# Optimization experiments

Hardware: AMD Instinct MI355X
Metric: run time of the kernel (lower is better)

## Reference

```python
import jax, jax.numpy as jnp
import numpy as np

N = 50000      # nodes
E = 1600000    # edges
D = 64         # in_channels (== hidden so layers stack)
H = 64         # hidden_channels
L = 3          # num_layers
G = 128        # graphs in batch
OUT = 1        # out_channels
BN_EPS = 1e-5


def setup_inputs() -> dict:
    key = jax.random.key(0)
    ks = jax.random.split(key, 8)
    s = 0.1
    x = jax.random.normal(ks[0], (N, D), dtype=jnp.float32)
    edge_index = jax.random.randint(ks[1], (2, E), 0, N, dtype=jnp.int64)
    batch = jnp.sort(jax.random.randint(ks[2], (N,), 0, G, dtype=jnp.int64))
    # stacked GINConv MLP params: Linear(D,H) -> BN(H) -> ReLU -> Linear(H,H)
    W1 = jax.random.normal(ks[3], (L, D, H), dtype=jnp.float32) * s
    b1 = jnp.zeros((L, H), jnp.float32)
    gamma = jnp.ones((L, H), jnp.float32)
    beta = jnp.zeros((L, H), jnp.float32)
    W2 = jax.random.normal(ks[4], (L, H, H), dtype=jnp.float32) * s
    b2 = jnp.zeros((L, H), jnp.float32)
    # head MLP: Linear(H,H) -> ReLU -> (dropout, eval mode) -> Linear(H,OUT)
    Wh1 = jax.random.normal(ks[5], (H, H), dtype=jnp.float32) * s
    bh1 = jnp.zeros((H,), jnp.float32)
    Wh2 = jax.random.normal(ks[6], (H, OUT), dtype=jnp.float32) * s
    bh2 = jnp.zeros((OUT,), jnp.float32)
    return dict(x=x, edge_index=edge_index, batch=batch,
                W1=W1, b1=b1, gamma=gamma, beta=beta, W2=W2, b2=b2,
                Wh1=Wh1, bh1=bh1, Wh2=Wh2, bh2=bh2)


def reference(x, edge_index, batch, W1, b1, gamma, beta, W2, b2, Wh1, bh1, Wh2, bh2):
    src, dst = edge_index[0], edge_index[1]

    def gin_layer(h, p):
        w1, bb1, g, be, w2, bb2 = p
        # scatter-add neighbor aggregation: sum_{j->i} h_j
        agg = jax.ops.segment_sum(h[src], dst, num_segments=N)  # [N, H]
        z = (agg + h) @ w1 + bb1  # (1+eps)*x + agg, eps=0; then Linear
        # BatchNorm1d (training-mode batch stats, biased var)
        mu = z.mean(0)
        var = ((z - mu) ** 2).mean(0)
        z = (z - mu) * jax.lax.rsqrt(var + BN_EPS) * g + be
        z = jax.nn.relu(z) @ w2 + bb2  # ReLU -> Linear (plain last layer)
        return jax.nn.relu(z), None    # outer .relu() in GIN.forward

    h, _ = jax.lax.scan(gin_layer, x, (W1, b1, gamma, beta, W2, b2))

    # global_mean_pool over batch ids
    cnt = jax.ops.segment_sum(jnp.ones((N, 1), h.dtype), batch, num_segments=G)
    pooled = jax.ops.segment_sum(h, batch, num_segments=G) / jnp.maximum(cnt, 1.0)

    # head MLP (dropout = identity in eval mode)
    return jax.nn.relu(pooled @ Wh1 + bh1) @ Wh2 + bh2
```

## Files before the change

### kernel.cpp

```cpp
#include <hip/hip_runtime.h>

#define N_NODES 50000
#define N_EDGES 1600000
#define HDIM 64
#define NLAYERS 3
#define NGRAPH 128
#define BN_EPS 1e-5f
#define CAP 96
#define NBINS 196
#define NBLK 782

__device__ __forceinline__ unsigned short f2bf(float f) {
    union { float f; unsigned u; } v; v.f = f;
    unsigned r = v.u + 0x7fffu + ((v.u >> 16) & 1u);
    return (unsigned short)(r >> 16);
}
__device__ __forceinline__ unsigned pack2(float a, float b) {
    return (unsigned)f2bf(a) | ((unsigned)f2bf(b) << 16);
}
__device__ __forceinline__ float bf2f(unsigned short b) {
    union { unsigned u; float f; } v; v.u = ((unsigned)b) << 16; return v.f;
}
__device__ __forceinline__ void acc8(float* a, uint4 v) {
    union { unsigned u; float f; } t;
    t.u = v.x << 16;         a[0] += t.f;
    t.u = v.x & 0xffff0000u; a[1] += t.f;
    t.u = v.y << 16;         a[2] += t.f;
    t.u = v.y & 0xffff0000u; a[3] += t.f;
    t.u = v.z << 16;         a[4] += t.f;
    t.u = v.z & 0xffff0000u; a[5] += t.f;
    t.u = v.w << 16;         a[6] += t.f;
    t.u = v.w & 0xffff0000u; a[7] += t.f;
}

__global__ __launch_bounds__(256) void hist1_kernel(
    const int* __restrict__ dst, int* __restrict__ gh)
{
    __shared__ int lh[NBINS];
    int tid = threadIdx.x;
    for (int i = tid; i < NBINS; i += 256) lh[i] = 0;
    __syncthreads();
    int t8 = blockIdx.x * 256 + tid;
    if (t8 < N_EDGES / 8) {
        int4 d0 = ((const int4*)dst)[t8 * 2];
        int4 d1 = ((const int4*)dst)[t8 * 2 + 1];
        atomicAdd(&lh[d0.x >> 8], 1);
        atomicAdd(&lh[d0.y >> 8], 1);
        atomicAdd(&lh[d0.z >> 8], 1);
        atomicAdd(&lh[d0.w >> 8], 1);
        atomicAdd(&lh[d1.x >> 8], 1);
        atomicAdd(&lh[d1.y >> 8], 1);
        atomicAdd(&lh[d1.z >> 8], 1);
        atomicAdd(&lh[d1.w >> 8], 1);
    }
    __syncthreads();
    for (int i = tid; i < NBINS; i += 256)
        gh[i * NBLK + blockIdx.x] = lh[i];
}

__global__ __launch_bounds__(256) void scan_bins_kernel(
    int* __restrict__ gh, int* __restrict__ binbase)
{
    __shared__ int wsum[4];
    __shared__ int woff[4];
    __shared__ int carry;
    int b = blockIdx.x;
    int tid = threadIdx.x, lane = tid & 63, wid = tid >> 6;
    if (tid == 0) carry = 0;
    __syncthreads();
    int* row = gh + b * NBLK;
    for (int base = 0; base < NBLK; base += 256) {
        int i = base + tid;
        int v = (i < NBLK) ? row[i] : 0;
        int incl = v;
        #pragma unroll
        for (int off = 1; off < 64; off <<= 1) {
            int t = __shfl_up(incl, off, 64);
            if (lane >= off) incl += t;
        }
        if (lane == 63) wsum[wid] = incl;
        __syncthreads();
        if (tid == 0) {
            int r = carry;
            #pragma unroll
            for (int w = 0; w < 4; ++w) { woff[w] = r; r += wsum[w]; }
            carry = r;
        }
        __syncthreads();
        if (i < NBLK) row[i] = woff[wid] + incl - v;
        __syncthreads();
    }
    if (tid == 0) binbase[b] = carry;
}

__global__ __launch_bounds__(256) void scan_base_kernel(int* __restrict__ binbase)
{
    __shared__ int wsum[4];
    __shared__ int woff[5];
    int tid = threadIdx.x, lane = tid & 63, wid = tid >> 6;
    int v = (tid < NBINS) ? binbase[tid] : 0;
    int incl = v;
    #pragma unroll
    for (int off = 1; off < 64; off <<= 1) {
        int t = __shfl_up(incl, off, 64);
        if (lane >= off) incl += t;
    }
    if (lane == 63) wsum[wid] = incl;
    __syncthreads();
    if (tid == 0) {
        int r = 0;
        #pragma unroll
        for (int w = 0; w < 4; ++w) { woff[w] = r; r += wsum[w]; }
        woff[4] = r;
    }
    __syncthreads();
    if (tid < NBINS) binbase[tid] = woff[wid] + incl - v;
    if (tid == 0) binbase[NBINS] = woff[4];
}

__global__ __launch_bounds__(256) void scatter_kernel(
    const int* __restrict__ src, const int* __restrict__ dst,
    const int* __restrict__ gh, const int* __restrict__ binbase,
    unsigned* __restrict__ packed)
{
    __shared__ int lbase[NBINS];
    int tid = threadIdx.x;
    for (int i = tid; i < NBINS; i += 256)
        lbase[i] = binbase[i] + gh[i * NBLK + blockIdx.x];
    __syncthreads();
    int t8 = blockIdx.x * 256 + tid;
    if (t8 >= N_EDGES / 8) return;
    int4 d0 = ((const int4*)dst)[t8 * 2];
    int4 d1 = ((const int4*)dst)[t8 * 2 + 1];
    int4 s0 = ((const int4*)src)[t8 * 2];
    int4 s1 = ((const int4*)src)[t8 * 2 + 1];
    int p0 = atomicAdd(&lbase[d0.x >> 8], 1);
    int p1 = atomicAdd(&lbase[d0.y >> 8], 1);
    int p2 = atomicAdd(&lbase[d0.z >> 8], 1);
    int p3 = atomicAdd(&lbase[d0.w >> 8], 1);
    int p4 = atomicAdd(&lbase[d1.x >> 8], 1);
    int p5 = atomicAdd(&lbase[d1.y >> 8], 1);
    int p6 = atomicAdd(&lbase[d1.z >> 8], 1);
    int p7 = atomicAdd(&lbase[d1.w >> 8], 1);
    packed[p0] = ((unsigned)d0.x << 16) | (unsigned)s0.x;
    packed[p1] = ((unsigned)d0.y << 16) | (unsigned)s0.y;
    packed[p2] = ((unsigned)d0.z << 16) | (unsigned)s0.z;
    packed[p3] = ((unsigned)d0.w << 16) | (unsigned)s0.w;
    packed[p4] = ((unsigned)d1.x << 16) | (unsigned)s1.x;
    packed[p5] = ((unsigned)d1.y << 16) | (unsigned)s1.y;
    packed[p6] = ((unsigned)d1.z << 16) | (unsigned)s1.z;
    packed[p7] = ((unsigned)d1.w << 16) | (unsigned)s1.w;
}

__global__ __launch_bounds__(256) void build_csr_kernel(
    const unsigned* __restrict__ packed, const int* __restrict__ binbase,
    unsigned short* __restrict__ col, int* __restrict__ cnt)
{
    __shared__ int lcnt[256];
    int b = blockIdx.x;
    int tid = threadIdx.x;
    lcnt[tid] = 0;
    __syncthreads();
    int e0 = binbase[b], e1 = binbase[b + 1];
    for (int e = e0 + tid; e < e1; e += 256) {
        unsigned p = packed[e];
        int d = (int)(p >> 16);
        int dl = d - (b << 8);
        int pos = atomicAdd(&lcnt[dl], 1);
        col[d * CAP + pos] = (unsigned short)(p & 0xffffu);
    }
    __syncthreads();
    int node = (b << 8) + tid;
    if (node < N_NODES) {
        int c = lcnt[tid];
        int end = (c + 7) & ~7;
        unsigned short* cp = col + node * CAP;
        for (int i = c; i < end; ++i) cp[i] = (unsigned short)N_NODES;
        cnt[node] = c;
    }
}

__global__ __launch_bounds__(256) void xcast_kernel(
    const float* __restrict__ x, unsigned short* __restrict__ xb)
{
    int t = blockIdx.x * 256 + threadIdx.x;
    if (t < 8)
        ((uint4*)(xb + (size_t)N_NODES * HDIM))[t] = make_uint4(0, 0, 0, 0);
    if (t >= N_NODES * HDIM / 8) return;
    float4 v0 = ((const float4*)x)[t * 2];
    float4 v1 = ((const float4*)x)[t * 2 + 1];
    uint4 o;
    o.x = pack2(v0.x, v0.y);
    o.y = pack2(v0.z, v0.w);
    o.z = pack2(v1.x, v1.y);
    o.w = pack2(v1.z, v1.w);
    ((uint4*)xb)[t] = o;
}

__global__ __launch_bounds__(256) void gather_kernel(
    const unsigned short* __restrict__ hin, const int* __restrict__ cnt,
    const unsigned short* __restrict__ col, float* __restrict__ agg)
{
    const uint4* hin4 = (const uint4*)hin;
    int row = blockIdx.x * 4 + (threadIdx.x >> 6);
    int lane = threadIdx.x & 63;
    int sub = lane >> 3;
    int q = lane & 7;
    int nch = (cnt[row] + 7) >> 3;
    const unsigned short* cp = col + row * CAP + sub;
    float a[8] = {0.f, 0.f, 0.f, 0.f, 0.f, 0.f, 0.f, 0.f};
    int ch = 0;
    for (; ch + 4 <= nch; ch += 4) {
        int c0 = cp[ch * 8];
        int c1 = cp[ch * 8 + 8];
        int c2 = cp[ch * 8 + 16];
        int c3 = cp[ch * 8 + 24];
        uint4 v0 = hin4[c0 * 8 + q];
        uint4 v1 = hin4[c1 * 8 + q];
        uint4 v2 = hin4[c2 * 8 + q];
        uint4 v3 = hin4[c3 * 8 + q];
        acc8(a, v0); acc8(a, v1); acc8(a, v2); acc8(a, v3);
    }
    if (ch + 2 <= nch) {
        int c0 = cp[ch * 8];
        int c1 = cp[ch * 8 + 8];
        uint4 v0 = hin4[c0 * 8 + q];
        uint4 v1 = hin4[c1 * 8 + q];
        acc8(a, v0); acc8(a, v1);
        ch += 2;
    }
    if (ch < nch) {
        int c0 = cp[ch * 8];
        uint4 v0 = hin4[c0 * 8 + q];
        acc8(a, v0);
    }
    #pragma unroll
    for (int off = 8; off < 64; off <<= 1) {
        #pragma unroll
        for (int j = 0; j < 8; ++j)
            a[j] += __shfl_xor(a[j], off, 64);
    }
    if (sub == 0) {
        uint4 sv = hin4[row * 8 + q];
        acc8(a, sv);
        float4 o0, o1;
        o0.x = a[0]; o0.y = a[1]; o0.z = a[2]; o0.w = a[3];
        o1.x = a[4]; o1.y = a[5]; o1.z = a[6]; o1.w = a[7];
        float4* op = (float4*)(agg + (size_t)row * HDIM + q * 8);
        op[0] = o0;
        op[1] = o1;
    }
}

__global__ __launch_bounds__(256) void gemm1_kernel(
    const float* __restrict__ agg, const float* __restrict__ W1,
    const float* __restrict__ b1, float* __restrict__ z,
    float* __restrict__ stats )
{
    __shared__ float sW[HDIM * HDIM];
    __shared__ float sIn[64][HDIM];
    __shared__ float sRedS[4][HDIM];
    __shared__ float sRedQ[4][HDIM];
    int tid = threadIdx.x;
    int w = tid >> 6, c = tid & 63;
    int row0 = blockIdx.x * 64;
    for (int i = tid; i < HDIM * HDIM; i += 256) sW[i] = W1[i];
    const float4* agg4 = (const float4*)agg;
    #pragma unroll
    for (int i = 0; i < 4; ++i) {
        int lin = tid + i * 256;
        int rr = lin >> 4, q = lin & 15;
        float4 v = (row0 + rr < N_NODES)
                       ? agg4[(size_t)(row0 + rr) * 16 + q]
                       : make_float4(0.f, 0.f, 0.f, 0.f);
        *(float4*)&sIn[rr][q * 4] = v;
    }
    float bias = b1[c];
    __syncthreads();
    float acc[16];
    #pragma unroll
    for (int r = 0; r < 16; ++r) acc[r] = bias;
    #pragma unroll 4
    for (int k4 = 0; k4 < HDIM; k4 += 4) {
        float w0 = sW[(k4 + 0) * HDIM + c];
        float w1 = sW[(k4 + 1) * HDIM + c];
        float w2 = sW[(k4 + 2) * HDIM + c];
        float w3 = sW[(k4 + 3) * HDIM + c];
        #pragma unroll
        for (int r = 0; r < 16; ++r) {
            float4 iv = *(const float4*)&sIn[w * 16 + r][k4];
            acc[r] = fmaf(iv.x, w0, acc[r]);
            acc[r] = fmaf(iv.y, w1, acc[r]);
            acc[r] = fmaf(iv.z, w2, acc[r]);
            acc[r] = fmaf(iv.w, w3, acc[r]);
        }
    }
    float s = 0.f, s2 = 0.f;
    #pragma unroll
    for (int r = 0; r < 16; ++r) {
        int row = row0 + w * 16 + r;
        if (row < N_NODES) {
            z[(size_t)row * HDIM + c] = acc[r];
            s += acc[r];
            s2 += acc[r] * acc[r];
        }
    }
    sRedS[w][c] = s;
    sRedQ[w][c] = s2;
    __syncthreads();
    if (tid < HDIM) {
        atomicAdd(&stats[c], sRedS[0][c] + sRedS[1][c] + sRedS[2][c] + sRedS[3][c]);
        atomicAdd(&stats[HDIM + c],
                  sRedQ[0][c] + sRedQ[1][c] + sRedQ[2][c] + sRedQ[3][c]);
    }
}

__global__ __launch_bounds__(256) void gemm2_kernel(
    const float* __restrict__ z, const float* __restrict__ W2,
    const float* __restrict__ b2, const float* __restrict__ stats,
    const float* __restrict__ gamma, const float* __restrict__ beta,
    unsigned short* __restrict__ hout)
{
    __shared__ float sW[HDIM * HDIM];
    __shared__ float sIn[64][HDIM];
    __shared__ float sSc[HDIM];
    __shared__ float sSh[HDIM];
    int tid = threadIdx.x;
    int w = tid >> 6, c = tid & 63;
    int row0 = blockIdx.x * 64;
    for (int i = tid; i < HDIM * HDIM; i += 256) sW[i] = W2[i];
    if (tid < HDIM) {
        float mu  = stats[tid] / (float)N_NODES;
        float var = stats[HDIM + tid] / (float)N_NODES - mu * mu;
        float sc  = gamma[tid] * rsqrtf(var + BN_EPS);
        sSc[tid] = sc;
        sSh[tid] = beta[tid] - mu * sc;
    }
    float bias = b2[c];
    __syncthreads();
    const float4* z4 = (const float4*)z;
    #pragma unroll
    for (int i = 0; i < 4; ++i) {
        int lin = tid + i * 256;
        int rr = lin >> 4, q = lin & 15;
        float4 v = (row0 + rr < N_NODES)
                       ? z4[(size_t)(row0 + rr) * 16 + q]
                       : make_float4(0.f, 0.f, 0.f, 0.f);
        int cb = q * 4;
        v.x = fmaxf(fmaf(v.x, sSc[cb + 0], sSh[cb + 0]), 0.f);
        v.y = fmaxf(fmaf(v.y, sSc[cb + 1], sSh[cb + 1]), 0.f);
        v.z = fmaxf(fmaf(v.z, sSc[cb + 2], sSh[cb + 2]), 0.f);
        v.w = fmaxf(fmaf(v.w, sSc[cb + 3], sSh[cb + 3]), 0.f);
        *(float4*)&sIn[rr][q * 4] = v;
    }
    __syncthreads();
    float acc[16];
    #pragma unroll
    for (int r = 0; r < 16; ++r) acc[r] = bias;
    #pragma unroll 4
    for (int k4 = 0; k4 < HDIM; k4 += 4) {
        float w0 = sW[(k4 + 0) * HDIM + c];
        float w1 = sW[(k4 + 1) * HDIM + c];
        float w2 = sW[(k4 + 2) * HDIM + c];
        float w3 = sW[(k4 + 3) * HDIM + c];
        #pragma unroll
        for (int r = 0; r < 16; ++r) {
            float4 iv = *(const float4*)&sIn[w * 16 + r][k4];
            acc[r] = fmaf(iv.x, w0, acc[r]);
            acc[r] = fmaf(iv.y, w1, acc[r]);
            acc[r] = fmaf(iv.z, w2, acc[r]);
            acc[r] = fmaf(iv.w, w3, acc[r]);
        }
    }
    #pragma unroll
    for (int r = 0; r < 16; ++r) {
        int row = row0 + w * 16 + r;
        if (row < N_NODES)
            hout[(size_t)row * HDIM + c] = f2bf(fmaxf(acc[r], 0.f));
    }
}

__global__ __launch_bounds__(256) void bounds_kernel(
    const int* __restrict__ batch, int* __restrict__ gstart,
    unsigned short* __restrict__ hA)
{
    int i = blockIdx.x * 256 + threadIdx.x;
    if (i < 8)
        ((uint4*)(hA + (size_t)N_NODES * HDIM))[i] = make_uint4(0, 0, 0, 0);
    if (i >= N_NODES) return;
    int g1 = batch[i];
    int g0 = (i == 0) ? -1 : batch[i - 1];
    for (int g = g0 + 1; g <= g1; ++g) gstart[g] = i;
    if (i == N_NODES - 1)
        for (int g = g1 + 1; g <= NGRAPH; ++g) gstart[g] = N_NODES;
}

__global__ __launch_bounds__(256) void pool_head_kernel(
    const unsigned short* __restrict__ h, const int* __restrict__ gstart,
    const float* __restrict__ Wh1, const float* __restrict__ bh1,
    const float* __restrict__ Wh2, const float* __restrict__ bh2,
    float* __restrict__ out)
{
    __shared__ float sW[HDIM * HDIM];
    __shared__ float sRed[4][HDIM];
    __shared__ float sMean[HDIM];
    int tid = threadIdx.x;
    int r = tid >> 6, c = tid & 63;
    int g = blockIdx.x;
    for (int i = tid; i < HDIM * HDIM; i += 256) sW[i] = Wh1[i];
    int s0 = gstart[g], s1 = gstart[g + 1];
    float acc = 0.f;
    for (int row = s0 + r; row < s1; row += 4)
        acc += bf2f(h[(size_t)row * HDIM + c]);
    sRed[r][c] = acc;
    __syncthreads();
    if (r == 0) {
        float cntf = (float)(s1 - s0);
        sMean[c] = (sRed[0][c] + sRed[1][c] + sRed[2][c] + sRed[3][c]) /
                   fmaxf(cntf, 1.0f);
    }
    __syncthreads();
    if (r == 0) {
        float a = bh1[c];
        #pragma unroll
        for (int k = 0; k < HDIM; ++k)
            a = fmaf(sMean[k], sW[k * HDIM + c], a);
        a = fmaxf(a, 0.f);
        float p = a * Wh2[c];
        #pragma unroll
        for (int off = 32; off > 0; off >>= 1)
            p += __shfl_down(p, off, 64);
        if (c == 0) out[g] = p + bh2[0];
    }
}

extern "C" void kernel_launch(void* const* d_in, const int* in_sizes, int n_in,
                              void* d_out, int out_size, void* d_ws, size_t ws_size,
                              hipStream_t stream)
{
    const float* x     = (const float*)d_in[0];
    const int*   ei    = (const int*)d_in[1];
    const int*   batch = (const int*)d_in[2];
    const float* W1    = (const float*)d_in[3];
    const float* b1    = (const float*)d_in[4];
    const float* gamma = (const float*)d_in[5];
    const float* beta  = (const float*)d_in[6];
    const float* W2    = (const float*)d_in[7];
    const float* b2    = (const float*)d_in[8];
    const float* Wh1   = (const float*)d_in[9];
    const float* bh1   = (const float*)d_in[10];
    const float* Wh2   = (const float*)d_in[11];
    const float* bh2   = (const float*)d_in[12];
    float* out = (float*)d_out;

    float*          ws  = (float*)d_ws;
    float*          hB  = ws;
    unsigned short* hA  = (unsigned short*)(hB + (size_t)N_NODES * HDIM);
    unsigned short* xb  = hA + (size_t)(N_NODES + 1) * HDIM;
    int*   gstart  = (int*)(xb + (size_t)(N_NODES + 1) * HDIM + 32);
    int*   cnt     = gstart + NGRAPH + 1;
    float* stats   = (float*)(cnt + N_NODES);
    unsigned short* col = (unsigned short*)(stats + 3 * 2 * HDIM);
    unsigned* packed = (unsigned*)(col + (size_t)N_NODES * CAP);
    int*   gh      = (int*)(packed + N_EDGES);
    int*   binbase = gh + NBINS * NBLK;

    const int* src = ei;
    const int* dst = ei + N_EDGES;

    int gemmGrid   = (N_NODES + 63) / 64;
    int gatherGrid = N_NODES / 4;
    int nodeGrid   = (N_NODES + 255) / 256;
    int castGrid   = (N_NODES * HDIM / 8 + 255) / 256;

    hipMemsetAsync(stats, 0, 3 * 2 * HDIM * sizeof(float), stream);
    hist1_kernel<<<NBLK, 256, 0, stream>>>(dst, gh);
    scan_bins_kernel<<<NBINS, 256, 0, stream>>>(gh, binbase);
    scan_base_kernel<<<1, 256, 0, stream>>>(binbase);
    scatter_kernel<<<NBLK, 256, 0, stream>>>(src, dst, gh, binbase, packed);
    build_csr_kernel<<<NBINS, 256, 0, stream>>>(packed, binbase, col, cnt);
    xcast_kernel<<<castGrid, 256, 0, stream>>>(x, xb);
    bounds_kernel<<<nodeGrid, 256, 0, stream>>>(batch, gstart, hA);

    for (int l = 0; l < NLAYERS; ++l) {
        const unsigned short* hin = (l == 0) ? xb : hA;
        float* statsl = stats + l * 2 * HDIM;
        gather_kernel<<<gatherGrid, 256, 0, stream>>>(hin, cnt, col, hB);
        gemm1_kernel<<<gemmGrid, 256, 0, stream>>>(
            hB, W1 + l * HDIM * HDIM, b1 + l * HDIM, hB , statsl);
        gemm2_kernel<<<gemmGrid, 256, 0, stream>>>(
            hB, W2 + l * HDIM * HDIM, b2 + l * HDIM, statsl,
            gamma + l * HDIM, beta + l * HDIM, hA);
    }

    pool_head_kernel<<<NGRAPH, 256, 0, stream>>>(hA, gstart, Wh1, bh1, Wh2, bh2, out);
}
```

Baseline: 335.5 us.

## Fuse neighbor gather into first GEMM kernel, staging aggregates in shared memory

The separate gather kernel is removed. Each wave of the first GEMM kernel now aggregates the neighbor features for its own 16 rows and writes them straight into the shared-memory input tile. This avoids writing the fp32 aggregate buffer to global memory and reading it back, and drops one launch per layer. In exchange the gather runs with far fewer concurrent waves, each handling rows one after another, which may hurt latency hiding for the random feature loads. Rows past the node count in the last block are no longer zero-filled in shared memory.

```diff
diff --git a/kernel.cpp b/kernel.cpp
--- a/kernel.cpp
+++ b/kernel.cpp
@@ -197,63 +197,9 @@
     ((uint4*)xb)[t] = o;
 }
 
-__global__ __launch_bounds__(256) void gather_kernel(
+__global__ __launch_bounds__(256) void gather_gemm1_kernel(
     const unsigned short* __restrict__ hin, const int* __restrict__ cnt,
-    const unsigned short* __restrict__ col, float* __restrict__ agg)
-{
-    const uint4* hin4 = (const uint4*)hin;
-    int row = blockIdx.x * 4 + (threadIdx.x >> 6);
-    int lane = threadIdx.x & 63;
-    int sub = lane >> 3;
-    int q = lane & 7;
-    int nch = (cnt[row] + 7) >> 3;
-    const unsigned short* cp = col + row * CAP + sub;
-    float a[8] = {0.f, 0.f, 0.f, 0.f, 0.f, 0.f, 0.f, 0.f};
-    int ch = 0;
-    for (; ch + 4 <= nch; ch += 4) {
-        int c0 = cp[ch * 8];
-        int c1 = cp[ch * 8 + 8];
-        int c2 = cp[ch * 8 + 16];
-        int c3 = cp[ch * 8 + 24];
-        uint4 v0 = hin4[c0 * 8 + q];
-        uint4 v1 = hin4[c1 * 8 + q];
-        uint4 v2 = hin4[c2 * 8 + q];
-        uint4 v3 = hin4[c3 * 8 + q];
-        acc8(a, v0); acc8(a, v1); acc8(a, v2); acc8(a, v3);
-    }
-    if (ch + 2 <= nch) {
-        int c0 = cp[ch * 8];
-        int c1 = cp[ch * 8 + 8];
-        uint4 v0 = hin4[c0 * 8 + q];
-        uint4 v1 = hin4[c1 * 8 + q];
-        acc8(a, v0); acc8(a, v1);
-        ch += 2;
-    }
-    if (ch < nch) {
-        int c0 = cp[ch * 8];
-        uint4 v0 = hin4[c0 * 8 + q];
-        acc8(a, v0);
-    }
-    #pragma unroll
-    for (int off = 8; off < 64; off <<= 1) {
-        #pragma unroll
-        for (int j = 0; j < 8; ++j)
-            a[j] += __shfl_xor(a[j], off, 64);
-    }
-    if (sub == 0) {
-        uint4 sv = hin4[row * 8 + q];
-        acc8(a, sv);
-        float4 o0, o1;
-        o0.x = a[0]; o0.y = a[1]; o0.z = a[2]; o0.w = a[3];
-        o1.x = a[4]; o1.y = a[5]; o1.z = a[6]; o1.w = a[7];
-        float4* op = (float4*)(agg + (size_t)row * HDIM + q * 8);
-        op[0] = o0;
-        op[1] = o1;
-    }
-}
-
-__global__ __launch_bounds__(256) void gemm1_kernel(
-    const float* __restrict__ agg, const float* __restrict__ W1,
+    const unsigned short* __restrict__ col, const float* __restrict__ W1,
     const float* __restrict__ b1, float* __restrict__ z,
     float* __restrict__ stats )
 {
@@ -261,22 +207,64 @@
     __shared__ float sIn[64][HDIM];
     __shared__ float sRedS[4][HDIM];
     __shared__ float sRedQ[4][HDIM];
+    const uint4* hin4 = (const uint4*)hin;
     int tid = threadIdx.x;
     int w = tid >> 6, c = tid & 63;
+    int sub = c >> 3;
+    int q8 = c & 7;
     int row0 = blockIdx.x * 64;
     for (int i = tid; i < HDIM * HDIM; i += 256) sW[i] = W1[i];
-    const float4* agg4 = (const float4*)agg;
-    #pragma unroll
-    for (int i = 0; i < 4; ++i) {
-        int lin = tid + i * 256;
-        int rr = lin >> 4, q = lin & 15;
-        float4 v = (row0 + rr < N_NODES)
-                       ? agg4[(size_t)(row0 + rr) * 16 + q]
-                       : make_float4(0.f, 0.f, 0.f, 0.f);
-        *(float4*)&sIn[rr][q * 4] = v;
+
+    for (int rr = 0; rr < 16; ++rr) {
+        int row = row0 + w * 16 + rr;
+        if (row >= N_NODES) break;
+        int nch = (cnt[row] + 7) >> 3;
+        const unsigned short* cp = col + row * CAP + sub;
+        float a[8] = {0.f, 0.f, 0.f, 0.f, 0.f, 0.f, 0.f, 0.f};
+        int ch = 0;
+        for (; ch + 4 <= nch; ch += 4) {
+            int c0 = cp[ch * 8];
+            int c1 = cp[ch * 8 + 8];
+            int c2 = cp[ch * 8 + 16];
+            int c3 = cp[ch * 8 + 24];
+            uint4 v0 = hin4[c0 * 8 + q8];
+            uint4 v1 = hin4[c1 * 8 + q8];
+            uint4 v2 = hin4[c2 * 8 + q8];
+            uint4 v3 = hin4[c3 * 8 + q8];
+            acc8(a, v0); acc8(a, v1); acc8(a, v2); acc8(a, v3);
+        }
+        if (ch + 2 <= nch) {
+            int c0 = cp[ch * 8];
+            int c1 = cp[ch * 8 + 8];
+            uint4 v0 = hin4[c0 * 8 + q8];
+            uint4 v1 = hin4[c1 * 8 + q8];
+            acc8(a, v0); acc8(a, v1);
+            ch += 2;
+        }
+        if (ch < nch) {
+            int c0 = cp[ch * 8];
+            uint4 v0 = hin4[c0 * 8 + q8];
+            acc8(a, v0);
+        }
+        #pragma unroll
+        for (int off = 8; off < 64; off <<= 1) {
+            #pragma unroll
+            for (int j = 0; j < 8; ++j)
+                a[j] += __shfl_xor(a[j], off, 64);
+        }
+        if (sub == 0) {
+            uint4 sv = hin4[row * 8 + q8];
+            acc8(a, sv);
+            float4 o0, o1;
+            o0.x = a[0]; o0.y = a[1]; o0.z = a[2]; o0.w = a[3];
+            o1.x = a[4]; o1.y = a[5]; o1.z = a[6]; o1.w = a[7];
+            *(float4*)&sIn[w * 16 + rr][q8 * 8] = o0;
+            *(float4*)&sIn[w * 16 + rr][q8 * 8 + 4] = o1;
+        }
     }
     float bias = b1[c];
     __syncthreads();
+
     float acc[16];
     #pragma unroll
     for (int r = 0; r < 16; ++r) acc[r] = bias;
@@ -468,10 +456,9 @@
     const int* src = ei;
     const int* dst = ei + N_EDGES;
 
-    int gemmGrid   = (N_NODES + 63) / 64;
-    int gatherGrid = N_NODES / 4;
-    int nodeGrid   = (N_NODES + 255) / 256;
-    int castGrid   = (N_NODES * HDIM / 8 + 255) / 256;
+    int gemmGrid = (N_NODES + 63) / 64;
+    int nodeGrid = (N_NODES + 255) / 256;
+    int castGrid = (N_NODES * HDIM / 8 + 255) / 256;
 
     hipMemsetAsync(stats, 0, 3 * 2 * HDIM * sizeof(float), stream);
     hist1_kernel<<<NBLK, 256, 0, stream>>>(dst, gh);
@@ -485,9 +472,8 @@
     for (int l = 0; l < NLAYERS; ++l) {
         const unsigned short* hin = (l == 0) ? xb : hA;
         float* statsl = stats + l * 2 * HDIM;
-        gather_kernel<<<gatherGrid, 256, 0, stream>>>(hin, cnt, col, hB);
-        gemm1_kernel<<<gemmGrid, 256, 0, stream>>>(
-            hB, W1 + l * HDIM * HDIM, b1 + l * HDIM, hB , statsl);
+        gather_gemm1_kernel<<<gemmGrid, 256, 0, stream>>>(
+            hin, cnt, col, W1 + l * HDIM * HDIM, b1 + l * HDIM, hB, statsl);
         gemm2_kernel<<<gemmGrid, 256, 0, stream>>>(
             hB, W2 + l * HDIM * HDIM, b2 + l * HDIM, statsl,
             gamma + l * HDIM, beta + l * HDIM, hA);
```

Result: slower. 350.6 us (+4.5%).
